# Optimization experiments

Hardware: AMD Instinct MI355X
Metric: run time of the kernel (lower is better)

## Reference

```python
import jax, jax.numpy as jnp
from jax import lax
import numpy as np

B, S, H, L = 128, 256, 768, 24


def setup_inputs() -> dict:
    key = jax.random.key(0)
    k_tf, k_len, k_w, k_tr, k_st, k_en = jax.random.split(key, 6)
    token_features = jax.random.normal(k_tf, (B, S, H), dtype=jnp.float32)
    # contiguous valid lengths in [3, S] (>=3 so that stripping CLS/SEP leaves >=1 token)
    lengths = jax.random.randint(k_len, (B,), 3, S + 1)
    pos = jnp.arange(S)
    input_mask = (pos[None, :] < lengths[:, None]).astype(jnp.int32)
    true_label_mask = (pos[None, :] < (lengths - 2)[:, None]).astype(jnp.int32)
    W = jax.random.normal(k_w, (H, L), dtype=jnp.float32) * 0.02
    b = jnp.zeros((L,), dtype=jnp.float32)
    transitions = jax.random.normal(k_tr, (L, L), dtype=jnp.float32) * 0.1
    start_trans = jax.random.normal(k_st, (L,), dtype=jnp.float32) * 0.1
    end_trans = jax.random.normal(k_en, (L,), dtype=jnp.float32) * 0.1
    return {
        "token_features": token_features,
        "input_mask": input_mask,
        "true_label_mask": true_label_mask,
        "W": W,
        "b": b,
        "transitions": transitions,
        "start_trans": start_trans,
        "end_trans": end_trans,
    }


def _compact(x, mask):
    """Vectorized version of the torch per-token copy loop: for each row,
    gather valid tokens (mask==1) preserving order, drop the first and last
    valid token (CLS/SEP), left-pack into a zero tensor."""
    # stable argsort puts valid positions first, in order
    order = jnp.argsort(1 - mask.astype(jnp.int32), axis=1)  # [B,S]
    gathered = jnp.take_along_axis(x, order[:, :, None], axis=1)  # [B,S,H]
    # drop first valid token (shift left by 1), pad a zero row at the end
    shifted = jnp.concatenate([gathered[:, 1:], jnp.zeros_like(gathered[:, :1])], axis=1)
    n_valid = mask.sum(axis=1)  # [B]
    keep = jnp.arange(x.shape[1])[None, :] < (n_valid[:, None] - 2)  # also drops last (SEP)
    return jnp.where(keep[:, :, None], shifted, 0.0)


def _viterbi(emissions, mask, transitions, start_trans, end_trans):
    """Masked Viterbi decode. emissions [B,S,L], mask [B,S] bool."""
    Bn, Sn, Ln = emissions.shape
    lbl = jnp.arange(Ln)
    score0 = start_trans[None, :] + emissions[:, 0]  # [B,L]

    def step(score, xs):
        em_t, m_t = xs  # [B,L], [B]
        cand = score[:, :, None] + transitions[None]  # [B,prev,curr]
        best = cand.max(axis=1) + em_t
        bp = cand.argmax(axis=1)  # [B,L] best prev tag per curr tag
        new_score = jnp.where(m_t[:, None], best, score)
        bp = jnp.where(m_t[:, None], bp, lbl[None, :])  # identity backpointer on pad
        return new_score, bp

    ems = jnp.swapaxes(emissions[:, 1:], 0, 1)  # [S-1,B,L]
    ms = jnp.swapaxes(mask[:, 1:], 0, 1)  # [S-1,B]
    final, bps = lax.scan(step, score0, (ems, ms))
    final = final + end_trans[None, :]
    best_score = final.max(axis=1)  # [B]
    last_tag = final.argmax(axis=1)  # [B]

    def back(tag, bp):  # tag: tag at time t; bp: bp_t -> tag at t-1
        prev = jnp.take_along_axis(bp, tag[:, None], axis=1)[:, 0]
        return prev, tag

    tag0, tags_rest = lax.scan(back, last_tag, bps, reverse=True)  # tags_rest [S-1,B]
    path = jnp.concatenate([tag0[:, None], jnp.swapaxes(tags_rest, 0, 1)], axis=1)  # [B,S]
    return best_score, path


def reference(token_features, input_mask, true_label_mask, W, b, transitions, start_trans, end_trans):
    mask = input_mask.astype(bool)
    wv = _compact(token_features, mask)  # dropout is identity at inference
    emissions = jax.nn.sigmoid(wv @ W + b)  # [B,S,L]
    _, path = _viterbi(emissions, true_label_mask != 0, transitions, start_trans, end_trans)
    return path
```

## Files before the change

kernel.cpp:

```cpp
#include <hip/hip_runtime.h>
#include <hip/hip_bf16.h>
#include <math.h>

#define NB 128
#define NS 256
#define NH 768
#define NL 24
#define ASTR 68
#define NW 10
#define SSTR 28

__global__ __launch_bounds__(256) void ner_emis(
    const float* __restrict__ tf, const int* __restrict__ tlm,
    const float* __restrict__ W, const float* __restrict__ bias,
    float* __restrict__ E)
{
    const int b    = blockIdx.x >> 3;
    const int tile = (blockIdx.x & 7) << 5;
    const int tid  = threadIdx.x;
    if (tlm[b*NS + tile] == 0) return;

    __shared__ float lds[8*32*25];
    float* As = lds;
    float* Ws = lds + 32*ASTR;
    float* Pr = lds;

    const int tok  = tid & 15;
    const int ksub = tid >> 4;
    const int kk   = ksub << 2;
    const int rot  = ksub & 3;

    float acc0[NL], acc1[NL];
    #pragma unroll
    for (int l = 0; l < NL; ++l) { acc0[l] = 0.f; acc1[l] = 0.f; }

    const float* tfb = tf + (size_t)(b*NS)*NH;

    for (int kc0 = 0; kc0 < NH; kc0 += 64) {
        #pragma unroll
        for (int i = 0; i < 2; ++i) {
            int idx  = tid + (i << 8);
            int row  = idx >> 4;
            int c4   = idx & 15;
            int trow = tile + row + 1;
            if (trow > 255) trow = 255;
            float4 v = *(const float4*)(tfb + (size_t)trow*NH + kc0 + (c4 << 2));
            float* dst = As + row*ASTR + (c4 << 2);
            dst[0] = v.x; dst[1] = v.y; dst[2] = v.z; dst[3] = v.w;
        }
        {
            const float4* wsrc = (const float4*)(W + (size_t)kc0*NL);
            float4* wdst = (float4*)Ws;
            for (int i = tid; i < 384; i += 256) wdst[i] = wsrc[i];
        }
        __syncthreads();

        const float* A0 = As + tok*ASTR + kk;
        const float* A1 = A0 + 16*ASTR;
        const float* Wr = Ws + kk*NL;
        #pragma unroll
        for (int s = 0; s < 4; ++s) {
            const int j = (s + rot) & 3;
            float a0 = A0[j];
            float a1 = A1[j];
            const float4* w4 = (const float4*)(Wr + j*NL);
            float wv[NL];
            #pragma unroll
            for (int i = 0; i < 6; ++i) {
                float4 w = w4[i];
                wv[4*i+0] = w.x; wv[4*i+1] = w.y; wv[4*i+2] = w.z; wv[4*i+3] = w.w;
            }
            #pragma unroll
            for (int l = 0; l < NL; ++l) {
                acc0[l] = fmaf(a0, wv[l], acc0[l]);
                acc1[l] = fmaf(a1, wv[l], acc1[l]);
            }
        }
        __syncthreads();
    }

    if (ksub >= 8) {
        float* p = Pr + ((ksub-8)*32 + tok)*25;
        float* q = p + 16*25;
        #pragma unroll
        for (int l = 0; l < NL; ++l) { p[l] = acc0[l]; q[l] = acc1[l]; }
    }
    __syncthreads();
    if (ksub < 8) {
        const float* p = Pr + (ksub*32 + tok)*25;
        const float* q = p + 16*25;
        #pragma unroll
        for (int l = 0; l < NL; ++l) { acc0[l] += p[l]; acc1[l] += q[l]; }
    }
    __syncthreads();
    if (ksub < 8) {
        float* p = Pr + (ksub*32 + tok)*25;
        float* q = p + 16*25;
        #pragma unroll
        for (int l = 0; l < NL; ++l) { p[l] = acc0[l]; q[l] = acc1[l]; }
    }
    __syncthreads();

    const int* tm = tlm + b*NS + tile;
    float* Eb = E + (size_t)(b*NS + tile)*NL;
    #pragma unroll
    for (int i = 0; i < 3; ++i) {
        int o = tid + (i << 8);
        int t = o / NL, l = o % NL;
        if (tm[t]) {
            float s = 0.f;
            #pragma unroll
            for (int ks = 0; ks < 8; ++ks)
                s += Pr[(ks*32 + t)*25 + l];
            float x = s + bias[l];
            Eb[t*NL + l] = 1.0f/(1.0f + expf(-x));
        }
    }
}

__global__ __launch_bounds__(256) void ner_viterbi(
    const float* __restrict__ E, const int* __restrict__ tlm,
    const float* __restrict__ trans, const float* __restrict__ st,
    const float* __restrict__ en, int* __restrict__ out)
{
    const int tid = threadIdx.x;
    const int b   = blockIdx.x;
    const int bS  = b*NS;

    __shared__ float Esh[262*NL];
    __shared__ float scl[NS*SSTR];
    __shared__ float Tt[NL*SSTR];
    __shared__ float fin[NL];
    __shared__ unsigned char tr_s[NL][NS];
    __shared__ int chosen[NW+2];
    __shared__ int nsh, ltag;

    {
        const float4* src = (const float4*)(E + (size_t)bS*NL);
        float4* dst = (float4*)Esh;
        #pragma unroll
        for (int j = 0; j < 6; ++j) dst[tid + (j << 8)] = src[tid + (j << 8)];
    }
    for (int i = tid; i < NL*NL; i += 256) {
        int c = i / NL, p = i % NL;
        Tt[c*SSTR + p] = trans[p*NL + c];
    }
    if (tid < 64) {
        int a = tlm[bS+tid] + tlm[bS+tid+64] + tlm[bS+tid+128] + tlm[bS+tid+192];
        #pragma unroll
        for (int off = 32; off > 0; off >>= 1) a += __shfl_down(a, off, 64);
        if (tid == 0) nsh = a;
    }
    __syncthreads();
    const int n = nsh;

    if (tid < 24) {
        const int c = tid;
        float Tc[NL];
        #pragma unroll
        for (int p = 0; p < NL; ++p) Tc[p] = trans[p*NL + c];

        float sv = st[c] + Esh[c];
        scl[c] = sv;

        auto step = [&](int t, float em) {
            const int svi = __float_as_int(sv);
            int rr[NL];
            #pragma unroll
            for (int p = 0; p < NL; ++p)
                rr[p] = __builtin_amdgcn_readlane(svi, p);
            __builtin_amdgcn_sched_barrier(0);
            float cand[NL];
            #pragma unroll
            for (int p = 0; p < NL; ++p)
                cand[p] = __int_as_float(rr[p]) + Tc[p];
            float m0 = fmaxf(fmaxf(cand[0],  cand[1]),  cand[2]);
            float m1 = fmaxf(fmaxf(cand[3],  cand[4]),  cand[5]);
            float m2 = fmaxf(fmaxf(cand[6],  cand[7]),  cand[8]);
            float m3 = fmaxf(fmaxf(cand[9],  cand[10]), cand[11]);
            float m4 = fmaxf(fmaxf(cand[12], cand[13]), cand[14]);
            float m5 = fmaxf(fmaxf(cand[15], cand[16]), cand[17]);
            float m6 = fmaxf(fmaxf(cand[18], cand[19]), cand[20]);
            float m7 = fmaxf(fmaxf(cand[21], cand[22]), cand[23]);
            float q0 = fmaxf(fmaxf(m0, m1), m2);
            float q1 = fmaxf(fmaxf(m3, m4), m5);
            float q2 = fmaxf(m6, m7);
            sv = fmaxf(fmaxf(q0, q1), q2) + em;
            scl[t*SSTR + c] = sv;
        };

        float emb[8];
        #pragma unroll
        for (int j = 0; j < 8; ++j) emb[j] = Esh[(1+j)*NL + c];
        int t0 = 1;
        for (; t0 + 8 <= n; t0 += 8) {
            float emc[8];
            #pragma unroll
            for (int j = 0; j < 8; ++j) emc[j] = emb[j];
            #pragma unroll
            for (int j = 0; j < 8; ++j) emb[j] = Esh[(t0+8+j)*NL + c];
            #pragma unroll
            for (int j = 0; j < 8; ++j) step(t0 + j, emc[j]);
        }
        for (; t0 < n; ++t0) step(t0, Esh[t0*NL + c]);
        fin[c] = sv + en[c];
    }
    __syncthreads();

    if (tid == 0) {
        float bv = fin[0]; int bt = 0;
        #pragma unroll
        for (int cc = 1; cc < 24; ++cc) { if (fin[cc] > bv) { bv = fin[cc]; bt = cc; } }
        ltag = bt;
    }
    __syncthreads();

    const int K = (n > 1) ? (n - 1 + NW - 1) / NW : 1;
    if (n > 1 && tid < NW*24) {
        const int w = tid / 24 + 1, h = tid % 24;
        int tlo = (w-1)*K; if (tlo > n-1) tlo = n-1;
        int thi = w*K;     if (thi > n-1) thi = n-1;
        int cur = h;
        for (int t = thi; t > tlo; --t) {
            const float4* sp = (const float4*)(scl + (t-1)*SSTR);
            const float4* up = (const float4*)(Tt + cur*SSTR);
            float cand[NL];
            #pragma unroll
            for (int i = 0; i < 6; ++i) {
                float4 s = sp[i], u = up[i];
                cand[4*i+0] = s.x + u.x;
                cand[4*i+1] = s.y + u.y;
                cand[4*i+2] = s.z + u.z;
                cand[4*i+3] = s.w + u.w;
            }
            float best = cand[0]; int arg = 0;
            #pragma unroll
            for (int p = 1; p < 24; ++p) { if (cand[p] > best) { best = cand[p]; arg = p; } }
            tr_s[h][t-1] = (unsigned char)arg;
            cur = arg;
        }
    }
    __syncthreads();

    if (tid == 0) {
        int cur = ltag;
        for (int w = NW; w >= 1; --w) {
            chosen[w] = cur;
            int tlo = (w-1)*K; if (tlo > n-1) tlo = n-1;
            int thi = w*K;     if (thi > n-1) thi = n-1;
            if (thi > tlo) cur = tr_s[cur][tlo];
        }
    }
    __syncthreads();

    {
        const int t = tid;
        int tag;
        if (t >= n-1) tag = ltag;
        else { int w = t / K + 1; tag = tr_s[chosen[w]][t]; }
        out[bS + t] = tag;
    }
}

extern "C" void kernel_launch(void* const* d_in, const int* in_sizes, int n_in,
                              void* d_out, int out_size, void* d_ws, size_t ws_size,
                              hipStream_t stream) {
    const float* tf    = (const float*)d_in[0];
    const int*   tlm   = (const int*)  d_in[2];
    const float* W     = (const float*)d_in[3];
    const float* bias  = (const float*)d_in[4];
    const float* trans = (const float*)d_in[5];
    const float* st    = (const float*)d_in[6];
    const float* en    = (const float*)d_in[7];
    float* E = (float*)d_ws;

    ner_emis<<<dim3(NB*8), dim3(256), 0, stream>>>(tf, tlm, W, bias, E);
    ner_viterbi<<<dim3(NB), dim3(256), 0, stream>>>(E, tlm, trans, st, en, (int*)d_out);
}
```

Baseline: 215.0 us.

## Retile emission GEMM to 64-token blocks and broadcast Viterbi scores via LDS

```diff
diff --git a/kernel.cpp b/kernel.cpp
--- a/kernel.cpp
+++ b/kernel.cpp
@@ -6,98 +6,88 @@
 #define NS 256
 #define NH 768
 #define NL 24
-#define ASTR 68
 #define NW 10
 #define SSTR 28
 
-__global__ __launch_bounds__(256) void ner_emis(
+__global__ __launch_bounds__(512) void ner_emis(
     const float* __restrict__ tf, const int* __restrict__ tlm,
     const float* __restrict__ W, const float* __restrict__ bias,
     float* __restrict__ E)
 {
-    const int b    = blockIdx.x >> 3;
-    const int tile = (blockIdx.x & 7) << 5;
+    const int b    = blockIdx.x >> 2;
+    const int tile = (blockIdx.x & 3) << 6;
     const int tid  = threadIdx.x;
     if (tlm[b*NS + tile] == 0) return;
 
-    __shared__ float lds[8*32*25];
+    __shared__ float lds[6400];
     float* As = lds;
-    float* Ws = lds + 32*ASTR;
+    float* Ws = lds + 64*65;
     float* Pr = lds;
 
-    const int tok  = tid & 15;
-    const int ksub = tid >> 4;
-    const int kk   = ksub << 2;
-    const int rot  = ksub & 3;
-
-    float acc0[NL], acc1[NL];
+    const int tok  = tid & 63;
+    const int ksub = tid >> 6;
+
+    float acc[NL];
     #pragma unroll
-    for (int l = 0; l < NL; ++l) { acc0[l] = 0.f; acc1[l] = 0.f; }
+    for (int l = 0; l < NL; ++l) acc[l] = 0.f;
 
     const float* tfb = tf + (size_t)(b*NS)*NH;
 
     for (int kc0 = 0; kc0 < NH; kc0 += 64) {
         #pragma unroll
         for (int i = 0; i < 2; ++i) {
-            int idx  = tid + (i << 8);
+            int idx  = tid + (i << 9);
             int row  = idx >> 4;
             int c4   = idx & 15;
             int trow = tile + row + 1;
             if (trow > 255) trow = 255;
             float4 v = *(const float4*)(tfb + (size_t)trow*NH + kc0 + (c4 << 2));
-            float* dst = As + row*ASTR + (c4 << 2);
+            float* dst = As + row*65 + (c4 << 2);
             dst[0] = v.x; dst[1] = v.y; dst[2] = v.z; dst[3] = v.w;
         }
-        {
-            const float4* wsrc = (const float4*)(W + (size_t)kc0*NL);
-            float4* wdst = (float4*)Ws;
-            for (int i = tid; i < 384; i += 256) wdst[i] = wsrc[i];
-        }
+        if (tid < 384) ((float4*)Ws)[tid] = ((const float4*)(W + (size_t)kc0*NL))[tid];
         __syncthreads();
 
-        const float* A0 = As + tok*ASTR + kk;
-        const float* A1 = A0 + 16*ASTR;
-        const float* Wr = Ws + kk*NL;
-        #pragma unroll
-        for (int s = 0; s < 4; ++s) {
-            const int j = (s + rot) & 3;
-            float a0 = A0[j];
-            float a1 = A1[j];
-            const float4* w4 = (const float4*)(Wr + j*NL);
-            float wv[NL];
-            #pragma unroll
-            for (int i = 0; i < 6; ++i) {
-                float4 w = w4[i];
-                wv[4*i+0] = w.x; wv[4*i+1] = w.y; wv[4*i+2] = w.z; wv[4*i+3] = w.w;
-            }
-            #pragma unroll
-            for (int l = 0; l < NL; ++l) {
-                acc0[l] = fmaf(a0, wv[l], acc0[l]);
-                acc1[l] = fmaf(a1, wv[l], acc1[l]);
-            }
+        const float* Arow = As + tok*65 + (ksub << 3);
+        #pragma unroll
+        for (int j = 0; j < 8; ++j) {
+            const int k = (ksub << 3) + j;
+            float a = Arow[j];
+            const float4* w4 = (const float4*)(Ws + k*NL);
+            float4 w0 = w4[0], w1 = w4[1], w2 = w4[2];
+            acc[0]  = fmaf(a, w0.x, acc[0]);  acc[1]  = fmaf(a, w0.y, acc[1]);
+            acc[2]  = fmaf(a, w0.z, acc[2]);  acc[3]  = fmaf(a, w0.w, acc[3]);
+            acc[4]  = fmaf(a, w1.x, acc[4]);  acc[5]  = fmaf(a, w1.y, acc[5]);
+            acc[6]  = fmaf(a, w1.z, acc[6]);  acc[7]  = fmaf(a, w1.w, acc[7]);
+            acc[8]  = fmaf(a, w2.x, acc[8]);  acc[9]  = fmaf(a, w2.y, acc[9]);
+            acc[10] = fmaf(a, w2.z, acc[10]); acc[11] = fmaf(a, w2.w, acc[11]);
+            float4 w3 = w4[3], w4v = w4[4], w5 = w4[5];
+            acc[12] = fmaf(a, w3.x, acc[12]); acc[13] = fmaf(a, w3.y, acc[13]);
+            acc[14] = fmaf(a, w3.z, acc[14]); acc[15] = fmaf(a, w3.w, acc[15]);
+            acc[16] = fmaf(a, w4v.x, acc[16]); acc[17] = fmaf(a, w4v.y, acc[17]);
+            acc[18] = fmaf(a, w4v.z, acc[18]); acc[19] = fmaf(a, w4v.w, acc[19]);
+            acc[20] = fmaf(a, w5.x, acc[20]); acc[21] = fmaf(a, w5.y, acc[21]);
+            acc[22] = fmaf(a, w5.z, acc[22]); acc[23] = fmaf(a, w5.w, acc[23]);
         }
         __syncthreads();
     }
 
-    if (ksub >= 8) {
-        float* p = Pr + ((ksub-8)*32 + tok)*25;
-        float* q = p + 16*25;
-        #pragma unroll
-        for (int l = 0; l < NL; ++l) { p[l] = acc0[l]; q[l] = acc1[l]; }
-    }
-    __syncthreads();
-    if (ksub < 8) {
-        const float* p = Pr + (ksub*32 + tok)*25;
-        const float* q = p + 16*25;
-        #pragma unroll
-        for (int l = 0; l < NL; ++l) { acc0[l] += p[l]; acc1[l] += q[l]; }
-    }
-    __syncthreads();
-    if (ksub < 8) {
-        float* p = Pr + (ksub*32 + tok)*25;
-        float* q = p + 16*25;
-        #pragma unroll
-        for (int l = 0; l < NL; ++l) { p[l] = acc0[l]; q[l] = acc1[l]; }
+    if (ksub >= 4) {
+        float* p = Pr + ((ksub-4)*64 + tok)*25;
+        #pragma unroll
+        for (int l = 0; l < NL; ++l) p[l] = acc[l];
+    }
+    __syncthreads();
+    if (ksub < 4) {
+        const float* p = Pr + (ksub*64 + tok)*25;
+        #pragma unroll
+        for (int l = 0; l < NL; ++l) acc[l] += p[l];
+    }
+    __syncthreads();
+    if (ksub < 4) {
+        float* p = Pr + (ksub*64 + tok)*25;
+        #pragma unroll
+        for (int l = 0; l < NL; ++l) p[l] = acc[l];
     }
     __syncthreads();
 
@@ -105,13 +95,11 @@
     float* Eb = E + (size_t)(b*NS + tile)*NL;
     #pragma unroll
     for (int i = 0; i < 3; ++i) {
-        int o = tid + (i << 8);
+        int o = tid + (i << 9);
         int t = o / NL, l = o % NL;
         if (tm[t]) {
-            float s = 0.f;
-            #pragma unroll
-            for (int ks = 0; ks < 8; ++ks)
-                s += Pr[(ks*32 + t)*25 + l];
+            float s = ((Pr[(0*64 + t)*25 + l] + Pr[(1*64 + t)*25 + l])
+                     +  Pr[(2*64 + t)*25 + l]) + Pr[(3*64 + t)*25 + l];
             float x = s + bias[l];
             Eb[t*NL + l] = 1.0f/(1.0f + expf(-x));
         }
@@ -131,6 +119,7 @@
     __shared__ float scl[NS*SSTR];
     __shared__ float Tt[NL*SSTR];
     __shared__ float fin[NL];
+    __shared__ __align__(16) float sbc[32];
     __shared__ unsigned char tr_s[NL][NS];
     __shared__ int chosen[NW+2];
     __shared__ int nsh, ltag;
@@ -162,18 +151,25 @@
 
         float sv = st[c] + Esh[c];
         scl[c] = sv;
+        const float4* sb4 = (const float4*)sbc;
 
         auto step = [&](int t, float em) {
-            const int svi = __float_as_int(sv);
-            int rr[NL];
-            #pragma unroll
-            for (int p = 0; p < NL; ++p)
-                rr[p] = __builtin_amdgcn_readlane(svi, p);
-            __builtin_amdgcn_sched_barrier(0);
+            sbc[c] = sv;
+            float4 s0 = sb4[0], s1 = sb4[1], s2 = sb4[2],
+                   s3 = sb4[3], s4 = sb4[4], s5 = sb4[5];
             float cand[NL];
-            #pragma unroll
-            for (int p = 0; p < NL; ++p)
-                cand[p] = __int_as_float(rr[p]) + Tc[p];
+            cand[0]  = s0.x + Tc[0];  cand[1]  = s0.y + Tc[1];
+            cand[2]  = s0.z + Tc[2];  cand[3]  = s0.w + Tc[3];
+            cand[4]  = s1.x + Tc[4];  cand[5]  = s1.y + Tc[5];
+            cand[6]  = s1.z + Tc[6];  cand[7]  = s1.w + Tc[7];
+            cand[8]  = s2.x + Tc[8];  cand[9]  = s2.y + Tc[9];
+            cand[10] = s2.z + Tc[10]; cand[11] = s2.w + Tc[11];
+            cand[12] = s3.x + Tc[12]; cand[13] = s3.y + Tc[13];
+            cand[14] = s3.z + Tc[14]; cand[15] = s3.w + Tc[15];
+            cand[16] = s4.x + Tc[16]; cand[17] = s4.y + Tc[17];
+            cand[18] = s4.z + Tc[18]; cand[19] = s4.w + Tc[19];
+            cand[20] = s5.x + Tc[20]; cand[21] = s5.y + Tc[21];
+            cand[22] = s5.z + Tc[22]; cand[23] = s5.w + Tc[23];
             float m0 = fmaxf(fmaxf(cand[0],  cand[1]),  cand[2]);
             float m1 = fmaxf(fmaxf(cand[3],  cand[4]),  cand[5]);
             float m2 = fmaxf(fmaxf(cand[6],  cand[7]),  cand[8]);
@@ -274,6 +270,6 @@
     const float* en    = (const float*)d_in[7];
     float* E = (float*)d_ws;
 
-    ner_emis<<<dim3(NB*8), dim3(256), 0, stream>>>(tf, tlm, W, bias, E);
+    ner_emis<<<dim3(NB*4), dim3(512), 0, stream>>>(tf, tlm, W, bias, E);
     ner_viterbi<<<dim3(NB), dim3(256), 0, stream>>>(E, tlm, trans, st, en, (int*)d_out);
 }
```

Result: faster. 210.2 us (-2.2%).
